# Kernel tuning notes

Measured on AMD Instinct MI355X. Metric: run time of the kernel, lower is better.

The kernel has to match this reference:

```python
import math
import jax, jax.numpy as jnp
import numpy as np

LMAX = 2


def _cg_complex(j1, m1, j2, m2, j3, m3):
    # Standard (Racah) Clebsch-Gordan coefficient <j1 m1 j2 m2 | j3 m3> for integer l.
    if m1 + m2 != m3 or j3 < abs(j1 - j2) or j3 > j1 + j2:
        return 0.0
    f = math.factorial
    pre = math.sqrt((2 * j3 + 1) * f(j3 + j1 - j2) * f(j3 - j1 + j2) * f(j1 + j2 - j3) / f(j1 + j2 + j3 + 1))
    pre *= math.sqrt(f(j3 + m3) * f(j3 - m3) * f(j1 - m1) * f(j1 + m1) * f(j2 - m2) * f(j2 + m2))
    kmin = max(0, j2 - j3 - m1, j1 + m2 - j3)
    kmax = min(j1 + j2 - j3, j1 - m1, j2 + m2)
    s = 0.0
    for k in range(kmin, kmax + 1):
        s += (-1.0) ** k / (f(k) * f(j1 + j2 - j3 - k) * f(j1 - m1 - k) * f(j2 + m2 - k) * f(j3 - j2 + m1 + k) * f(j3 - j1 - m2 + k))
    return pre * s


def _u_matrix(l):
    # Unitary map from complex SH (Condon-Shortley) to real SH, rows = real mu, cols = complex m.
    U = np.zeros((2 * l + 1, 2 * l + 1), dtype=np.complex128)
    U[l, l] = 1.0
    isq2 = 1.0 / math.sqrt(2.0)
    for m in range(1, l + 1):
        U[l + m, l - m] = isq2
        U[l + m, l + m] = ((-1.0) ** m) * isq2
        U[l - m, l - m] = 1j * isq2
        U[l - m, l + m] = -1j * ((-1.0) ** m) * isq2
    return U


def _real_clebsch_gordan(lmax):
    # Dense real-SH CG tensor over combined s=(l,m) indices, shape [S,S,S], S=(lmax+1)^2.
    S = (lmax + 1) ** 2
    cg = np.zeros((S, S, S))
    for l1 in range(lmax + 1):
        for l2 in range(lmax + 1):
            for l3 in range(abs(l1 - l2), min(lmax, l1 + l2) + 1):
                blk = np.zeros((2 * l1 + 1, 2 * l2 + 1, 2 * l3 + 1))
                for i1, m1 in enumerate(range(-l1, l1 + 1)):
                    for i2, m2 in enumerate(range(-l2, l2 + 1)):
                        for i3, m3 in enumerate(range(-l3, l3 + 1)):
                            blk[i1, i2, i3] = _cg_complex(l1, m1, l2, m2, l3, m3)
                U1, U2, U3 = _u_matrix(l1), _u_matrix(l2), _u_matrix(l3)
                r = np.einsum('am,bn,co,mno->abc', U1, U2, U3.conj(), blk.astype(np.complex128))
                r = r.real if (l1 + l2 + l3) % 2 == 0 else r.imag  # parity-dependent real part
                cg[l1 * l1:(l1 + 1) ** 2, l2 * l2:(l2 + 1) ** 2, l3 * l3:(l3 + 1) ** 2] = r
    return cg


def _sparse_cg(lmax):
    cg = _real_clebsch_gordan(lmax)
    i1, i2, i3 = np.nonzero(np.abs(cg) > 1e-10)
    vals = cg[i1, i2, i3].astype(np.float32)
    widx = np.floor(np.sqrt(i3.astype(np.float64))).astype(np.int32)  # l of output combined index
    return vals, i1.astype(np.int32), i2.astype(np.int32), i3.astype(np.int32), widx


def _spherical_harmonics_l2(d):
    # Real SH up to l=2, 'component' normalization (|x|=1 assumed). Order: (l,m) = (0,0),(1,-1),(1,0),(1,1),(2,-2..2).
    x, y, z = d[..., 0], d[..., 1], d[..., 2]
    s3, s5, s15 = math.sqrt(3.0), math.sqrt(5.0), math.sqrt(15.0)
    return jnp.stack([
        jnp.ones_like(x),
        s3 * y, s3 * z, s3 * x,
        s15 * x * y, s15 * y * z, 0.5 * s5 * (3.0 * z * z - 1.0), s15 * x * z, 0.5 * s15 * (x * x - y * y),
    ], axis=-1)


def setup_inputs():
    N_ATOMS, N_EDGES, N_BASIS, N_RADIAL = 1200, 12000, 128, 20
    S = (LMAX + 1) ** 2
    key = jax.random.key(0)
    ks = jax.random.split(key, 8)
    vals, i1, i2, i3, widx = _sparse_cg(LMAX)
    return {
        'x': jax.random.normal(ks[0], (N_ATOMS, S, N_BASIS), jnp.float32),
        'radial_ij': jax.random.uniform(ks[1], (N_EDGES, N_RADIAL), jnp.float32),
        'dir_ij': jax.random.normal(ks[2], (N_EDGES, 3), jnp.float32),
        'cutoff_ij': jax.random.uniform(ks[3], (N_EDGES, 1), jnp.float32),
        'W_filter': jax.random.normal(ks[6], (N_RADIAL, N_BASIS * (LMAX + 1)), jnp.float32) / math.sqrt(N_RADIAL),
        'b_filter': jnp.zeros((N_BASIS * (LMAX + 1),), jnp.float32),
        'cg_vals': jnp.asarray(vals),
        'idx_i': jax.random.randint(ks[4], (N_EDGES,), 0, N_ATOMS),
        'idx_j': jax.random.randint(ks[5], (N_EDGES,), 0, N_ATOMS),
        'cg_idx_in1': jnp.asarray(i1),
        'cg_idx_in2': jnp.asarray(i2),
        'cg_idx_out': jnp.asarray(i3),
        'w_idx': jnp.asarray(widx),
    }


def reference(x, radial_ij, dir_ij, cutoff_ij, W_filter, b_filter, cg_vals,
              idx_i, idx_j, cg_idx_in1, cg_idx_in2, cg_idx_out, w_idx):
    n_atoms, S, F = x.shape
    E = dir_ij.shape[0]
    d = dir_ij / jnp.linalg.norm(dir_ij, axis=-1, keepdims=True)
    Y = _spherical_harmonics_l2(d)                        # [E, S]
    Wij = (radial_ij @ W_filter + b_filter) * cutoff_ij   # [E, (lmax+1)*F]
    Wij = Wij.reshape(E, LMAX + 1, F)                     # per-l radial filter
    xj = x[idx_j]                                         # [E, S, F] neighbor features
    # Sparse CG tensor-product contraction over combined (l,m) indices.
    v = (Y[:, cg_idx_in2, None] * cg_vals[None, :, None]
         * Wij[:, w_idx, :] * xj[:, cg_idx_in1, :])       # [E, n_cg, F]
    yij = jnp.zeros((E, S, F), v.dtype).at[:, cg_idx_out, :].add(v)
    return jax.ops.segment_sum(yij, idx_i, num_segments=n_atoms)
```

## Files before the change

### kernel.cpp

```cpp
#include <hip/hip_runtime.h>
#include <math.h>


#define S9     9
#define MROW   12
#define NF     128
#define NRAD   20
#define CEDGE  8
#define MAXA   2048

__device__ inline float2 f2fma(float a, float2 b, float2 c) {
    return make_float2(fmaf(a, b.x, c.x), fmaf(a, b.y, c.y));
}

__global__ __launch_bounds__(1024) void csr_kernel(
    const int* __restrict__ idx_i, int E, int A, int max_chunks,
    int* __restrict__ offsets,
    int* __restrict__ chunk_off,
    int* __restrict__ chunk_atom,
    int* __restrict__ esorted,
    float* __restrict__ out)
{
    __shared__ int lcnt[MAXA];
    __shared__ int lcur[MAXA];
    __shared__ int part[1024];
    __shared__ int nch_sh;
    const int t = threadIdx.x;

    for (int i = t; i < A; i += 1024) lcnt[i] = 0;
    __syncthreads();
    for (int e = t; e < E; e += 1024) atomicAdd(&lcnt[idx_i[e]], 1);
    __syncthreads();

    const int i0 = 2 * t, i1 = 2 * t + 1;
    const int ca = (i0 < A) ? lcnt[i0] : 0;
    const int cb = (i1 < A) ? lcnt[i1] : 0;

    part[t] = ca + cb;
    __syncthreads();
    for (int off = 1; off < 1024; off <<= 1) {
        int v = (t >= off) ? part[t - off] : 0;
        __syncthreads();
        part[t] += v;
        __syncthreads();
    }
    int run = part[t] - (ca + cb);
    if (i0 < A) { offsets[i0] = run; lcur[i0] = run; run += ca; }
    if (i1 < A) { offsets[i1] = run; lcur[i1] = run; run += cb; }
    if (t == 1023) offsets[A] = run;
    __syncthreads();

    const int ka = (i0 < A) ? ((ca + CEDGE - 1) / CEDGE) : 0;
    const int kb = (i1 < A) ? ((cb + CEDGE - 1) / CEDGE) : 0;
    part[t] = ka + kb;
    __syncthreads();
    for (int off = 1; off < 1024; off <<= 1) {
        int v = (t >= off) ? part[t - off] : 0;
        __syncthreads();
        part[t] += v;
        __syncthreads();
    }
    int run2 = part[t] - (ka + kb);
    if (i0 < A) {
        chunk_off[i0] = run2;
        for (int k = 0; k < ka; ++k) chunk_atom[run2 + k] = i0;
        run2 += ka;
    }
    if (i1 < A) {
        chunk_off[i1] = run2;
        for (int k = 0; k < kb; ++k) chunk_atom[run2 + k] = i1;
        run2 += kb;
    }
    if (t == 1023) { chunk_off[A] = run2; nch_sh = run2; }

    const float4 z4 = make_float4(0.f, 0.f, 0.f, 0.f);
    if (i0 < A && ca == 0) {
        float4* o = (float4*)(out + (size_t)i0 * (S9 * NF));
        for (int s = 0; s < S9 * NF / 4; ++s) o[s] = z4;
    }
    if (i1 < A && cb == 0) {
        float4* o = (float4*)(out + (size_t)i1 * (S9 * NF));
        for (int s = 0; s < S9 * NF / 4; ++s) o[s] = z4;
    }
    __syncthreads();

    for (int i = nch_sh + t; i < max_chunks; i += 1024) chunk_atom[i] = -1;

    for (int e = t; e < E; e += 1024) {
        int p = atomicAdd(&lcur[idx_i[e]], 1);
        esorted[p] = e;
    }
}

__global__ __launch_bounds__(64) void so3_chunk_kernel(
    const float* __restrict__ x,
    const float* __restrict__ radial,
    const float* __restrict__ dir,
    const float* __restrict__ cutoff,
    const float* __restrict__ Wf,
    const float* __restrict__ bf,
    const float* __restrict__ cg_vals,
    const int* __restrict__ idx_j,
    const int* __restrict__ cg_i1,
    const int* __restrict__ cg_i2,
    const int* __restrict__ cg_i3,
    int ncg, int A,
    const int* __restrict__ offsets,
    const int* __restrict__ chunk_off,
    const int* __restrict__ chunk_atom,
    const int* __restrict__ esorted,
    float* __restrict__ slots,
    float* __restrict__ out,
    int use_slots)
{
    const int ch = blockIdx.x;
    const int a = chunk_atom[ch];
    if (a < 0) return;

    const int c0ch = chunk_off[a];
    const int nch  = chunk_off[a + 1] - c0ch;
    const int estart = offsets[a] + (ch - c0ch) * CEDGE;
    const int n = min(CEDGE, offsets[a + 1] - estart);

    const int t = threadIdx.x;

    __shared__ __align__(16) float M[CEDGE][MROW * S9];
    __shared__ float Ysh[CEDGE][S9];
    __shared__ float radsh[CEDGE][NRAD];
    __shared__ float cutsh[CEDGE];
    __shared__ float wsh[CEDGE][3][NF];
    __shared__ int   jsh[CEDGE];

    {
        float4* Mz = (float4*)&M[0][0];
        const int tot4 = CEDGE * MROW * S9 / 4;
        for (int qq = t; qq < tot4; qq += 64) Mz[qq] = make_float4(0.f, 0.f, 0.f, 0.f);
    }
    if (t < CEDGE) {
        int jj = a;
        float cut = 0.f;
        if (t < n) {
            const int e = esorted[estart + t];
            jj = idx_j[e];
            cut = cutoff[e];
            float dx = dir[3 * e], dy = dir[3 * e + 1], dz = dir[3 * e + 2];
            const float inv = rsqrtf(dx * dx + dy * dy + dz * dz);
            dx *= inv; dy *= inv; dz *= inv;
            const float s3c  = 1.7320508075688772f;
            const float s5c  = 2.2360679774997896f;
            const float s15c = 3.8729833462074170f;
            Ysh[t][0] = 1.0f;
            Ysh[t][1] = s3c * dy;
            Ysh[t][2] = s3c * dz;
            Ysh[t][3] = s3c * dx;
            Ysh[t][4] = s15c * dx * dy;
            Ysh[t][5] = s15c * dy * dz;
            Ysh[t][6] = 0.5f * s5c * (3.0f * dz * dz - 1.0f);
            Ysh[t][7] = s15c * dx * dz;
            Ysh[t][8] = 0.5f * s15c * (dx * dx - dy * dy);
        }
        jsh[t] = jj;
        cutsh[t] = cut;
    }
    for (int qq = t; qq < CEDGE * NRAD; qq += 64) {
        const int c = qq / NRAD;
        const int r = qq - c * NRAD;
        radsh[c][r] = (c < n) ? radial[(size_t)esorted[estart + c] * NRAD + r] : 0.f;
    }
    __syncthreads();

    {
        const float2 b0 = ((const float2*)(bf + 0 * NF))[t];
        const float2 b1 = ((const float2*)(bf + 1 * NF))[t];
        const float2 b2 = ((const float2*)(bf + 2 * NF))[t];
        float2 w[CEDGE][3];
        #pragma unroll
        for (int c = 0; c < CEDGE; ++c) { w[c][0] = b0; w[c][1] = b1; w[c][2] = b2; }
        #pragma unroll 4
        for (int r = 0; r < NRAD; ++r) {
            const float2* wrow = (const float2*)(Wf + r * (3 * NF));
            const float2 w0 = wrow[t];
            const float2 w1 = wrow[t + 64];
            const float2 w2 = wrow[t + 128];
            #pragma unroll
            for (int c = 0; c < CEDGE; ++c) {
                const float rv = radsh[c][r];
                w[c][0] = f2fma(rv, w0, w[c][0]);
                w[c][1] = f2fma(rv, w1, w[c][1]);
                w[c][2] = f2fma(rv, w2, w[c][2]);
            }
        }
        #pragma unroll
        for (int c = 0; c < CEDGE; ++c) {
            const float cut = cutsh[c];
            ((float2*)&wsh[c][0][0])[t] = make_float2(w[c][0].x * cut, w[c][0].y * cut);
            ((float2*)&wsh[c][1][0])[t] = make_float2(w[c][1].x * cut, w[c][1].y * cut);
            ((float2*)&wsh[c][2][0])[t] = make_float2(w[c][2].x * cut, w[c][2].y * cut);
        }
    }

    {
        const int c = t >> 3;
        const int r = t & 7;
        if (c < n) {
            for (int kk = r; kk < ncg; kk += 8) {
                atomicAdd(&M[c][cg_i3[kk] * MROW + cg_i1[kk]], cg_vals[kk] * Ysh[c][cg_i2[kk]]);
            }
        }
    }
    __syncthreads();

    float2 acc[S9];
    #pragma unroll
    for (int s = 0; s < S9; ++s) acc[s] = make_float2(0.f, 0.f);

    #pragma unroll
    for (int c = 0; c < CEDGE; ++c) {
        const int j = __builtin_amdgcn_readfirstlane(jsh[c]);

        const float2* xp = (const float2*)(x + (size_t)j * (S9 * NF)) + t;
        float2 xj[S9];
        #pragma unroll
        for (int s = 0; s < S9; ++s) xj[s] = xp[s * 64];

        const float2* wp = (const float2*)&wsh[c][0][0] + t;
        const float2 wl0 = wp[0];
        const float2 wl1 = wp[64];
        const float2 wl2 = wp[128];

        #pragma unroll
        for (int s3 = 0; s3 < S9; ++s3) {
            const float4* mr = (const float4*)&M[c][s3 * MROW];
            const float4 m0 = mr[0];
            const float4 m1 = mr[1];
            const float  m8 = M[c][s3 * MROW + 8];
            float2 tsum = make_float2(0.f, 0.f);
            tsum = f2fma(m0.x, xj[0], tsum);
            tsum = f2fma(m0.y, xj[1], tsum);
            tsum = f2fma(m0.z, xj[2], tsum);
            tsum = f2fma(m0.w, xj[3], tsum);
            tsum = f2fma(m1.x, xj[4], tsum);
            tsum = f2fma(m1.y, xj[5], tsum);
            tsum = f2fma(m1.z, xj[6], tsum);
            tsum = f2fma(m1.w, xj[7], tsum);
            tsum = f2fma(m8,   xj[8], tsum);
            const float2 wl = (s3 == 0) ? wl0 : ((s3 < 4) ? wl1 : wl2);
            acc[s3].x = fmaf(wl.x, tsum.x, acc[s3].x);
            acc[s3].y = fmaf(wl.y, tsum.y, acc[s3].y);
        }
    }

    if (!use_slots) {
        float* op = out + (size_t)a * (S9 * NF) + 2 * t;
        #pragma unroll
        for (int s = 0; s < S9; ++s) {
            atomicAdd(&op[s * NF],     acc[s].x);
            atomicAdd(&op[s * NF + 1], acc[s].y);
        }
        return;
    }

    if (nch == 1) {
        float2* op = (float2*)(out + (size_t)a * (S9 * NF)) + t;
        #pragma unroll
        for (int s = 0; s < S9; ++s) op[s * 64] = acc[s];
    } else {
        float2* sp = (float2*)(slots + (size_t)ch * (S9 * NF)) + t;
        #pragma unroll
        for (int s = 0; s < S9; ++s) sp[s * 64] = acc[s];
    }
}

__global__ __launch_bounds__(64) void so3_reduce_kernel(
    const float* __restrict__ slots, const int* __restrict__ chunk_off,
    float* __restrict__ out)
{
    const int a = blockIdx.x;
    const int t = threadIdx.x;
    const int c0 = chunk_off[a];
    const int c1 = chunk_off[a + 1];
    if (c1 - c0 < 2) return;

    float2 acc[S9];
    #pragma unroll
    for (int s = 0; s < S9; ++s) acc[s] = make_float2(0.f, 0.f);

    for (int ch = c0; ch < c1; ++ch) {
        const float2* sp = (const float2*)(slots + (size_t)ch * (S9 * NF)) + t;
        #pragma unroll
        for (int s = 0; s < S9; ++s) {
            float2 v = sp[s * 64];
            acc[s].x += v.x; acc[s].y += v.y;
        }
    }
    float2* op = (float2*)(out + (size_t)a * (S9 * NF)) + t;
    #pragma unroll
    for (int s = 0; s < S9; ++s) op[s * 64] = acc[s];
}

extern "C" void kernel_launch(void* const* d_in, const int* in_sizes, int n_in,
                              void* d_out, int out_size, void* d_ws, size_t ws_size,
                              hipStream_t stream) {
    const float* x       = (const float*)d_in[0];
    const float* radial  = (const float*)d_in[1];
    const float* dir     = (const float*)d_in[2];
    const float* cutoff  = (const float*)d_in[3];
    const float* Wf      = (const float*)d_in[4];
    const float* bf      = (const float*)d_in[5];
    const float* cg_vals = (const float*)d_in[6];
    const int*   idx_i   = (const int*)d_in[7];
    const int*   idx_j   = (const int*)d_in[8];
    const int*   cg_i1   = (const int*)d_in[9];
    const int*   cg_i2   = (const int*)d_in[10];
    const int*   cg_i3   = (const int*)d_in[11];

    const int E   = in_sizes[7];
    const int ncg = in_sizes[6];
    const int A   = in_sizes[0] / (S9 * NF);

    const int max_chunks = E / CEDGE + A;

    int* offsets    = (int*)d_ws;
    int* chunk_off  = offsets + (A + 1);
    int* chunk_atom = chunk_off + (A + 1);
    int* esorted    = chunk_atom + max_chunks;
    size_t int_bytes = (size_t)(2 * A + 2 + max_chunks + E) * sizeof(int);
    size_t slots_off = (int_bytes + 255) & ~(size_t)255;

    size_t slots_bytes = (size_t)max_chunks * (S9 * NF) * sizeof(float);
    const int use_slots = (ws_size >= slots_off + slots_bytes) ? 1 : 0;
    float* slots = (float*)((char*)d_ws + slots_off);
    float* out   = (float*)d_out;

    if (!use_slots) {
        hipMemsetAsync(out, 0, (size_t)out_size * sizeof(float), stream);
    }

    csr_kernel<<<1, 1024, 0, stream>>>(idx_i, E, A, max_chunks,
                                       offsets, chunk_off, chunk_atom, esorted, out);

    so3_chunk_kernel<<<max_chunks, 64, 0, stream>>>(
        x, radial, dir, cutoff, Wf, bf, cg_vals, idx_j,
        cg_i1, cg_i2, cg_i3, ncg, A, offsets, chunk_off, chunk_atom, esorted,
        slots, out, use_slots);

    if (use_slots) {
        so3_reduce_kernel<<<A, 64, 0, stream>>>(slots, chunk_off, out);
    }
}
```

Baseline: 125.2 us.

## Halve edges per chunk, keep radial filter in registers, use wave-shuffle CSR scan

Halves the number of edges per block chunk (CEDGE 8 to 4), so more blocks run and each does less serial work. The per-edge radial filter now stays in registers instead of going through shared memory. The CSR build kernel replaces two block-wide shared-memory Hillis-Steele scans with a single wave-shuffle scan over a packed 64-bit (count, chunk) pair, which needs far fewer barriers. The trade-off is more chunks, and therefore more atomic or slot reductions per atom; the CG-matrix build now uses 16 threads per edge.

```diff
diff --git a/kernel.cpp b/kernel.cpp
--- a/kernel.cpp
+++ b/kernel.cpp
@@ -6,7 +6,7 @@
 #define MROW   12
 #define NF     128
 #define NRAD   20
-#define CEDGE  8
+#define CEDGE  4
 #define MAXA   2048
 
 __device__ inline float2 f2fma(float a, float2 b, float2 c) {
@@ -23,9 +23,11 @@
 {
     __shared__ int lcnt[MAXA];
     __shared__ int lcur[MAXA];
-    __shared__ int part[1024];
+    __shared__ unsigned long long wtot[16];
     __shared__ int nch_sh;
     const int t = threadIdx.x;
+    const int lane = t & 63;
+    const int wid  = t >> 6;
 
     for (int i = t; i < A; i += 1024) lcnt[i] = 0;
     __syncthreads();
@@ -35,43 +37,51 @@
     const int i0 = 2 * t, i1 = 2 * t + 1;
     const int ca = (i0 < A) ? lcnt[i0] : 0;
     const int cb = (i1 < A) ? lcnt[i1] : 0;
-
-    part[t] = ca + cb;
-    __syncthreads();
-    for (int off = 1; off < 1024; off <<= 1) {
-        int v = (t >= off) ? part[t - off] : 0;
-        __syncthreads();
-        part[t] += v;
-        __syncthreads();
-    }
-    int run = part[t] - (ca + cb);
-    if (i0 < A) { offsets[i0] = run; lcur[i0] = run; run += ca; }
-    if (i1 < A) { offsets[i1] = run; lcur[i1] = run; run += cb; }
-    if (t == 1023) offsets[A] = run;
-    __syncthreads();
-
     const int ka = (i0 < A) ? ((ca + CEDGE - 1) / CEDGE) : 0;
     const int kb = (i1 < A) ? ((cb + CEDGE - 1) / CEDGE) : 0;
-    part[t] = ka + kb;
-    __syncthreads();
-    for (int off = 1; off < 1024; off <<= 1) {
-        int v = (t >= off) ? part[t - off] : 0;
-        __syncthreads();
-        part[t] += v;
-        __syncthreads();
-    }
-    int run2 = part[t] - (ka + kb);
+
+    const unsigned long long mine =
+        (unsigned long long)(unsigned)(ca + cb) |
+        ((unsigned long long)(unsigned)(ka + kb) << 32);
+    unsigned long long inc = mine;
+    #pragma unroll
+    for (int d = 1; d < 64; d <<= 1) {
+        unsigned long long u = __shfl_up(inc, d);
+        if (lane >= d) inc += u;
+    }
+    if (lane == 63) wtot[wid] = inc;
+    __syncthreads();
+    if (wid == 0) {
+        unsigned long long w = (lane < 16) ? wtot[lane] : 0ull;
+        #pragma unroll
+        for (int d = 1; d < 16; d <<= 1) {
+            unsigned long long u = __shfl_up(w, d);
+            if (lane >= d) w += u;
+        }
+        if (lane < 16) wtot[lane] = w;
+    }
+    __syncthreads();
+    const unsigned long long wpre = (wid > 0) ? wtot[wid - 1] : 0ull;
+    const unsigned long long exc  = wpre + (inc - mine);
+
+    int run  = (int)(exc & 0xffffffffull);
+    int run2 = (int)(exc >> 32);
     if (i0 < A) {
-        chunk_off[i0] = run2;
+        offsets[i0] = run; lcur[i0] = run; chunk_off[i0] = run2;
         for (int k = 0; k < ka; ++k) chunk_atom[run2 + k] = i0;
-        run2 += ka;
+        run += ca; run2 += ka;
     }
     if (i1 < A) {
-        chunk_off[i1] = run2;
+        offsets[i1] = run; lcur[i1] = run; chunk_off[i1] = run2;
         for (int k = 0; k < kb; ++k) chunk_atom[run2 + k] = i1;
-        run2 += kb;
-    }
-    if (t == 1023) { chunk_off[A] = run2; nch_sh = run2; }
+        run += cb; run2 += kb;
+    }
+    if (t == 1023) {
+        const unsigned long long g = wtot[15];
+        offsets[A]   = (int)(g & 0xffffffffull);
+        chunk_off[A] = (int)(g >> 32);
+        nch_sh       = (int)(g >> 32);
+    }
 
     const float4 z4 = make_float4(0.f, 0.f, 0.f, 0.f);
     if (i0 < A && ca == 0) {
@@ -128,7 +138,6 @@
     __shared__ float Ysh[CEDGE][S9];
     __shared__ float radsh[CEDGE][NRAD];
     __shared__ float cutsh[CEDGE];
-    __shared__ float wsh[CEDGE][3][NF];
     __shared__ int   jsh[CEDGE];
 
     {
@@ -169,11 +178,11 @@
     }
     __syncthreads();
 
+    float2 w[CEDGE][3];
     {
         const float2 b0 = ((const float2*)(bf + 0 * NF))[t];
         const float2 b1 = ((const float2*)(bf + 1 * NF))[t];
         const float2 b2 = ((const float2*)(bf + 2 * NF))[t];
-        float2 w[CEDGE][3];
         #pragma unroll
         for (int c = 0; c < CEDGE; ++c) { w[c][0] = b0; w[c][1] = b1; w[c][2] = b2; }
         #pragma unroll 4
@@ -193,17 +202,17 @@
         #pragma unroll
         for (int c = 0; c < CEDGE; ++c) {
             const float cut = cutsh[c];
-            ((float2*)&wsh[c][0][0])[t] = make_float2(w[c][0].x * cut, w[c][0].y * cut);
-            ((float2*)&wsh[c][1][0])[t] = make_float2(w[c][1].x * cut, w[c][1].y * cut);
-            ((float2*)&wsh[c][2][0])[t] = make_float2(w[c][2].x * cut, w[c][2].y * cut);
+            w[c][0].x *= cut; w[c][0].y *= cut;
+            w[c][1].x *= cut; w[c][1].y *= cut;
+            w[c][2].x *= cut; w[c][2].y *= cut;
         }
     }
 
     {
-        const int c = t >> 3;
-        const int r = t & 7;
+        const int c = t >> 4;
+        const int r = t & 15;
         if (c < n) {
-            for (int kk = r; kk < ncg; kk += 8) {
+            for (int kk = r; kk < ncg; kk += 16) {
                 atomicAdd(&M[c][cg_i3[kk] * MROW + cg_i1[kk]], cg_vals[kk] * Ysh[c][cg_i2[kk]]);
             }
         }
@@ -222,11 +231,6 @@
         float2 xj[S9];
         #pragma unroll
         for (int s = 0; s < S9; ++s) xj[s] = xp[s * 64];
-
-        const float2* wp = (const float2*)&wsh[c][0][0] + t;
-        const float2 wl0 = wp[0];
-        const float2 wl1 = wp[64];
-        const float2 wl2 = wp[128];
 
         #pragma unroll
         for (int s3 = 0; s3 < S9; ++s3) {
@@ -244,7 +248,7 @@
             tsum = f2fma(m1.z, xj[6], tsum);
             tsum = f2fma(m1.w, xj[7], tsum);
             tsum = f2fma(m8,   xj[8], tsum);
-            const float2 wl = (s3 == 0) ? wl0 : ((s3 < 4) ? wl1 : wl2);
+            const float2 wl = (s3 == 0) ? w[c][0] : ((s3 < 4) ? w[c][1] : w[c][2]);
             acc[s3].x = fmaf(wl.x, tsum.x, acc[s3].x);
             acc[s3].y = fmaf(wl.y, tsum.y, acc[s3].y);
         }
```

Measured after the change: 124.5 us. No clear change (-0.6%).
